# Kernel optimization log

Measured on AMD Instinct MI355X. Metric: run time of the kernel, lower is better.

Reference implementation:

```python
import jax, jax.numpy as jnp
import numpy as np

B, Z, A, D = 2048, 128, 4, 50000
EPS = 1e-8


def setup_inputs() -> dict:
    key = jax.random.key(0)
    k1, k2, k3, k4, k5 = jax.random.split(key, 5)
    return {
        "batch_x": jax.random.normal(k1, (B, Z), dtype=jnp.float32),
        "batch_next": jax.random.normal(k2, (B, Z), dtype=jnp.float32),
        "keys": jax.random.normal(k3, (A, D, Z), dtype=jnp.float32),
        "vals": jax.random.normal(k4, (A, D, Z), dtype=jnp.float32),
        "batch_a": jax.random.randint(k5, (B,), 0, A, dtype=jnp.int64),
    }


def _dnd_lookup(q, keys_a, vals_a):
    # q: [B, Z] (L2-normalized), keys_a: [D, Z], vals_a: [D, Z]
    kn = keys_a / (jnp.linalg.norm(keys_a, axis=-1, keepdims=True) + EPS)
    sims = jnp.einsum("bz,dz->bd", q, kn)          # cosine similarity [B, D]
    w = jax.nn.softmax(sims, axis=-1)                # attention over dictionary
    return jnp.einsum("bd,dz->bz", w, vals_a)       # [B, Z]


def reference(batch_x, batch_next, keys, vals, batch_a):
    # Per-sample routed DND lookup: each sample queries the memory of its action,
    # then MSE loss vs batch_next (eval-mode trainBatch; memory write is a state
    # mutation done after the loss and does not affect the returned value).
    qn = batch_x / (jnp.linalg.norm(batch_x, axis=-1, keepdims=True) + EPS)
    a_space = keys.shape[0]
    pred = jnp.zeros_like(batch_x)
    for a in range(a_space):  # small fixed loop over distinct memories
        pred_a = _dnd_lookup(qn, keys[a], vals[a])
        pred = jnp.where((batch_a == a)[:, None], pred_a, pred)
    return jnp.mean((pred - batch_next) ** 2)
```

## Files before the change

### kernel.cpp

```cpp
#include <hip/hip_runtime.h>
#include <stdint.h>

#define B_N 2048
#define Z_N 128
#define A_N 4
#define D_N 50000
#define EPS_F 1e-8f

typedef __attribute__((ext_vector_type(8))) short short8;
typedef __attribute__((ext_vector_type(4))) float f32x4;

__device__ __forceinline__ unsigned short f2bf(float f) {
  unsigned int u = __builtin_bit_cast(unsigned int, f);
  u += 0x7FFFu + ((u >> 16) & 1u);
  return (unsigned short)(u >> 16);
}

__global__ void k_qnorm_route(const float* __restrict__ x, const int* __restrict__ act,
                              float* __restrict__ qn, int* __restrict__ counts,
                              int* __restrict__ lists) {
  int w = threadIdx.x >> 6, lane = threadIdx.x & 63;
  int row = blockIdx.x * 4 + w;
  const float2 v = ((const float2*)(x + (size_t)row * Z_N))[lane];
  float ss = v.x * v.x + v.y * v.y;
#pragma unroll
  for (int m = 1; m < 64; m <<= 1) ss += __shfl_xor(ss, m);
  float inv = 1.0f / (sqrtf(ss) + EPS_F);
  float2 o; o.x = v.x * inv; o.y = v.y * inv;
  ((float2*)(qn + (size_t)row * Z_N))[lane] = o;
  if (lane == 0) {
    int a = act[row];
    int pos = atomicAdd(&counts[a], 1);
    lists[a * B_N + pos] = row;
  }
}

__global__ void k_keynorm(const float* __restrict__ keys, unsigned short* __restrict__ kn) {
  int w = threadIdx.x >> 6, lane = threadIdx.x & 63;
  size_t row = (size_t)blockIdx.x * 4 + w;
  const float2 v = ((const float2*)(keys + row * Z_N))[lane];
  float ss = v.x * v.x + v.y * v.y;
#pragma unroll
  for (int m = 1; m < 64; m <<= 1) ss += __shfl_xor(ss, m);
  float inv = 1.0f / (sqrtf(ss) + EPS_F);
  unsigned short2_t;
  unsigned int packed = ((unsigned int)f2bf(v.y * inv) << 16) | f2bf(v.x * inv);
  ((unsigned int*)(kn + row * Z_N))[lane] = packed;
}

__global__ void k_vtrans(const float* __restrict__ vals, unsigned short* __restrict__ vt) {
  __shared__ float tile[64][65];
  int a = blockIdx.z, d0 = blockIdx.x * 64, z0 = blockIdx.y * 64;
  int t = threadIdx.x;
  int r = t >> 4, c4 = (t & 15) * 4;
#pragma unroll
  for (int i = 0; i < 4; ++i) {
    int dr = r + i * 16, d = d0 + dr;
    if (d < D_N) {
      const float4 v = *(const float4*)(vals + ((size_t)a * D_N + d) * Z_N + z0 + c4);
      tile[dr][c4 + 0] = v.x; tile[dr][c4 + 1] = v.y;
      tile[dr][c4 + 2] = v.z; tile[dr][c4 + 3] = v.w;
    }
  }
  __syncthreads();
  int zz = t >> 2, dg = (t & 3) * 16;
  if (d0 + dg < D_N) {
    union { unsigned short u[16]; uint4 q[2]; } pk;
#pragma unroll
    for (int j = 0; j < 16; ++j) pk.u[j] = f2bf(tile[dg + j][zz]);
    unsigned short* dst = vt + ((size_t)a * Z_N + z0 + zz) * D_N + d0 + dg;
    ((uint4*)dst)[0] = pk.q[0];
    ((uint4*)dst)[1] = pk.q[1];
  }
}

#define TILE_B 128
#define KT 32
#define CHUNK 1568
#define NITER 49

__launch_bounds__(256, 2)
__global__ void k_flash(const unsigned short* __restrict__ kn,
                        const unsigned short* __restrict__ vt,
                        const float* __restrict__ qn,
                        const int* __restrict__ counts,
                        const int* __restrict__ lists,
                        float* __restrict__ acc,
                        float* __restrict__ sume) {
  int a = blockIdx.z, ty = blockIdx.y;
  int nb = counts[a];
  if (ty * TILE_B >= nb) return;

  __shared__ unsigned short Kl[KT * 136];
  __shared__ unsigned short Vl[128 * 40];
  __shared__ unsigned short Pl[4][32 * 40];

  int t = threadIdx.x;
  int w = t >> 6, lane = t & 63;
  int lq = lane >> 4, ln = lane & 15;

  const unsigned short* kn_a = kn + (size_t)a * D_N * Z_N;
  const unsigned short* vt_a = vt + (size_t)a * Z_N * D_N;
  const int* list_a = lists + a * B_N;

  short8 qf[2][4];
#pragma unroll
  for (int mt = 0; mt < 2; ++mt) {
    int g = ty * TILE_B + w * 32 + mt * 16 + ln;
    bool valid = g < nb;
    int si = valid ? list_a[g] : 0;
#pragma unroll
    for (int c = 0; c < 4; ++c) {
      float4 f0 = {0.f, 0.f, 0.f, 0.f}, f1 = {0.f, 0.f, 0.f, 0.f};
      if (valid) {
        const float* qp = qn + (size_t)si * Z_N + c * 32 + lq * 8;
        f0 = *(const float4*)qp;
        f1 = *(const float4*)(qp + 4);
      }
      short8 s;
      s[0] = (short)f2bf(f0.x); s[1] = (short)f2bf(f0.y);
      s[2] = (short)f2bf(f0.z); s[3] = (short)f2bf(f0.w);
      s[4] = (short)f2bf(f1.x); s[5] = (short)f2bf(f1.y);
      s[6] = (short)f2bf(f1.z); s[7] = (short)f2bf(f1.w);
      qf[mt][c] = s;
    }
  }

  f32x4 O[2][8];
#pragma unroll
  for (int mt = 0; mt < 2; ++mt)
#pragma unroll
    for (int zt = 0; zt < 8; ++zt) O[mt][zt] = (f32x4){0.f, 0.f, 0.f, 0.f};
  float rs[2][4] = {{0.f, 0.f, 0.f, 0.f}, {0.f, 0.f, 0.f, 0.f}};

  int d_base = blockIdx.x * CHUNK;
  int sk_key = t >> 3, sk_z = (t & 7) * 16;
  int sv_z = t >> 1, sv_k = (t & 1) * 16;

  for (int kt = 0; kt < NITER; ++kt) {
    int d0 = d_base + kt * KT;
    if (d0 >= D_N) break;
    __syncthreads();
    {
      int key = d0 + sk_key;
      if (key < D_N) {
        const uint4* src = (const uint4*)(kn_a + (size_t)key * Z_N + sk_z);
        uint4* dst = (uint4*)&Kl[sk_key * 136 + sk_z];
        dst[0] = src[0]; dst[1] = src[1];
      }
    }
    {
      int kk = d0 + sv_k;
      const unsigned short* src = vt_a + (size_t)sv_z * D_N + kk;
      uint4* dst = (uint4*)&Vl[sv_z * 40 + sv_k];
      if (kk < D_N)     dst[0] = *(const uint4*)src;
      if (kk + 8 < D_N) dst[1] = *(const uint4*)(src + 8);
    }
    __syncthreads();

    f32x4 S[2][2];
#pragma unroll
    for (int nt = 0; nt < 2; ++nt) {
      short8 kf[4];
#pragma unroll
      for (int c = 0; c < 4; ++c)
        kf[c] = *(const short8*)&Kl[(nt * 16 + ln) * 136 + c * 32 + lq * 8];
#pragma unroll
      for (int mt = 0; mt < 2; ++mt) {
        f32x4 s4 = (f32x4){0.f, 0.f, 0.f, 0.f};
#pragma unroll
        for (int c = 0; c < 4; ++c)
          s4 = __builtin_amdgcn_mfma_f32_16x16x32_bf16(qf[mt][c], kf[c], s4, 0, 0, 0);
        S[mt][nt] = s4;
      }
    }

#pragma unroll
    for (int mt = 0; mt < 2; ++mt)
#pragma unroll
      for (int nt = 0; nt < 2; ++nt) {
        bool kv = (d0 + nt * 16 + ln) < D_N;
#pragma unroll
        for (int r = 0; r < 4; ++r) {
          float e = kv ? __expf(S[mt][nt][r]) : 0.f;
          rs[mt][r] += e;
          Pl[w][(mt * 16 + lq * 4 + r) * 40 + nt * 16 + ln] = f2bf(e);
        }
      }

    short8 pf0 = *(const short8*)&Pl[w][(ln) * 40 + lq * 8];
    short8 pf1 = *(const short8*)&Pl[w][(16 + ln) * 40 + lq * 8];
#pragma unroll
    for (int zt = 0; zt < 8; ++zt) {
      short8 vf = *(const short8*)&Vl[(zt * 16 + ln) * 40 + lq * 8];
      O[0][zt] = __builtin_amdgcn_mfma_f32_16x16x32_bf16(pf0, vf, O[0][zt], 0, 0, 0);
      O[1][zt] = __builtin_amdgcn_mfma_f32_16x16x32_bf16(pf1, vf, O[1][zt], 0, 0, 0);
    }
  }

#pragma unroll
  for (int mt = 0; mt < 2; ++mt)
#pragma unroll
    for (int r = 0; r < 4; ++r) {
      float v = rs[mt][r];
      v += __shfl_xor(v, 1); v += __shfl_xor(v, 2);
      v += __shfl_xor(v, 4); v += __shfl_xor(v, 8);
      rs[mt][r] = v;
    }

#pragma unroll
  for (int mt = 0; mt < 2; ++mt)
#pragma unroll
    for (int r = 0; r < 4; ++r) {
      int g = ty * TILE_B + w * 32 + mt * 16 + lq * 4 + r;
      if (g < nb) {
        int si = list_a[g];
        float* arow = acc + (size_t)si * Z_N + ln;
#pragma unroll
        for (int zt = 0; zt < 8; ++zt) atomicAdd(arow + zt * 16, O[mt][zt][r]);
        if (ln == 0) atomicAdd(&sume[si], rs[mt][r]);
      }
    }
}

__global__ void k_loss(const float* __restrict__ acc, const float* __restrict__ sume,
                       const float* __restrict__ nxt, float* __restrict__ loss) {
  int w = threadIdx.x >> 6, lane = threadIdx.x & 63;
  int row = blockIdx.x * 4 + w;
  float inv = 1.0f / sume[row];
  const float2 p2 = ((const float2*)(acc + (size_t)row * Z_N))[lane];
  const float2 n2 = ((const float2*)(nxt + (size_t)row * Z_N))[lane];
  float dx = p2.x * inv - n2.x, dy = p2.y * inv - n2.y;
  float s = dx * dx + dy * dy;
#pragma unroll
  for (int m = 1; m < 64; m <<= 1) s += __shfl_xor(s, m);
  if (lane == 0) atomicAdd(loss, s);
}

__global__ void k_final(const float* __restrict__ loss, float* __restrict__ out) {
  out[0] = loss[0] * (1.0f / (float)(B_N * Z_N));
}

extern "C" void kernel_launch(void* const* d_in, const int* in_sizes, int n_in,
                              void* d_out, int out_size, void* d_ws, size_t ws_size,
                              hipStream_t stream) {
  const float* x    = (const float*)d_in[0];
  const float* nxt  = (const float*)d_in[1];
  const float* keys = (const float*)d_in[2];
  const float* vals = (const float*)d_in[3];
  const int*   act  = (const int*)d_in[4];

  char* ws = (char*)d_ws;
  float* qn     = (float*)(ws + 0);
  float* acc    = (float*)(ws + 1048576);
  float* sume   = (float*)(ws + 2097152);
  int*   counts = (int*)(ws + 2105344);
  float* loss   = (float*)(ws + 2105360);
  int*   lists  = (int*)(ws + 2105376);
  unsigned short* kn = (unsigned short*)(ws + 2138368);
  unsigned short* vt = (unsigned short*)(ws + 53338368);

  hipMemsetAsync(ws + 1048576, 0, 1056800, stream);

  k_qnorm_route<<<512, 256, 0, stream>>>(x, act, qn, counts, lists);
  k_keynorm<<<50000, 256, 0, stream>>>(keys, kn);
  k_vtrans<<<dim3(782, 2, A_N), 256, 0, stream>>>(vals, vt);
  k_flash<<<dim3(32, 16, A_N), 256, 0, stream>>>(kn, vt, qn, counts, lists, acc, sume);
  k_loss<<<512, 256, 0, stream>>>(acc, sume, nxt, loss);
  k_final<<<1, 1, 0, stream>>>(loss, (float*)d_out);
}
```

Before: 435.3 us.

## Prefetch next K/V tile into registers and split dictionary into smaller chunks

```diff
diff --git a/kernel.cpp b/kernel.cpp
--- a/kernel.cpp
+++ b/kernel.cpp
@@ -43,7 +43,6 @@
 #pragma unroll
   for (int m = 1; m < 64; m <<= 1) ss += __shfl_xor(ss, m);
   float inv = 1.0f / (sqrtf(ss) + EPS_F);
-  unsigned short2_t;
   unsigned int packed = ((unsigned int)f2bf(v.y * inv) << 16) | f2bf(v.x * inv);
   ((unsigned int*)(kn + row * Z_N))[lane] = packed;
 }
@@ -76,10 +75,11 @@
 
 #define TILE_B 128
 #define KT 32
-#define CHUNK 1568
-#define NITER 49
-
-__launch_bounds__(256, 2)
+#define CHUNK 800
+#define NITER 25
+#define NCHUNK 63
+
+__launch_bounds__(256, 4)
 __global__ void k_flash(const unsigned short* __restrict__ kn,
                         const unsigned short* __restrict__ vt,
                         const float* __restrict__ qn,
@@ -137,26 +137,43 @@
   int sk_key = t >> 3, sk_z = (t & 7) * 16;
   int sv_z = t >> 1, sv_k = (t & 1) * 16;
 
+  const uint4 z4 = {0u, 0u, 0u, 0u};
+  uint4 kA, kB, vA, vB;
+
+  {
+    int key = d_base + sk_key;
+    bool kok = key < D_N;
+    const uint4* ksrc = (const uint4*)(kn_a + (size_t)key * Z_N + sk_z);
+    kA = kok ? ksrc[0] : z4;
+    kB = kok ? ksrc[1] : z4;
+    int kk = d_base + sv_k;
+    const unsigned short* vsrc = vt_a + (size_t)sv_z * D_N + kk;
+    vA = (kk < D_N)     ? *(const uint4*)vsrc       : z4;
+    vB = (kk + 8 < D_N) ? *(const uint4*)(vsrc + 8) : z4;
+  }
+
   for (int kt = 0; kt < NITER; ++kt) {
     int d0 = d_base + kt * KT;
-    if (d0 >= D_N) break;
     __syncthreads();
     {
-      int key = d0 + sk_key;
-      if (key < D_N) {
-        const uint4* src = (const uint4*)(kn_a + (size_t)key * Z_N + sk_z);
-        uint4* dst = (uint4*)&Kl[sk_key * 136 + sk_z];
-        dst[0] = src[0]; dst[1] = src[1];
-      }
-    }
-    {
-      int kk = d0 + sv_k;
-      const unsigned short* src = vt_a + (size_t)sv_z * D_N + kk;
-      uint4* dst = (uint4*)&Vl[sv_z * 40 + sv_k];
-      if (kk < D_N)     dst[0] = *(const uint4*)src;
-      if (kk + 8 < D_N) dst[1] = *(const uint4*)(src + 8);
+      uint4* kd = (uint4*)&Kl[sk_key * 136 + sk_z];
+      kd[0] = kA; kd[1] = kB;
+      uint4* vd = (uint4*)&Vl[sv_z * 40 + sv_k];
+      vd[0] = vA; vd[1] = vB;
     }
     __syncthreads();
+    if (kt + 1 < NITER) {
+      int d1 = d0 + KT;
+      int key = d1 + sk_key;
+      bool kok = key < D_N;
+      const uint4* ksrc = (const uint4*)(kn_a + (size_t)key * Z_N + sk_z);
+      kA = kok ? ksrc[0] : z4;
+      kB = kok ? ksrc[1] : z4;
+      int kk = d1 + sv_k;
+      const unsigned short* vsrc = vt_a + (size_t)sv_z * D_N + kk;
+      vA = (kk < D_N)     ? *(const uint4*)vsrc       : z4;
+      vB = (kk + 8 < D_N) ? *(const uint4*)(vsrc + 8) : z4;
+    }
 
     f32x4 S[2][2];
 #pragma unroll
@@ -225,6 +242,7 @@
 
 __global__ void k_loss(const float* __restrict__ acc, const float* __restrict__ sume,
                        const float* __restrict__ nxt, float* __restrict__ loss) {
+  __shared__ float ls[4];
   int w = threadIdx.x >> 6, lane = threadIdx.x & 63;
   int row = blockIdx.x * 4 + w;
   float inv = 1.0f / sume[row];
@@ -234,7 +252,9 @@
   float s = dx * dx + dy * dy;
 #pragma unroll
   for (int m = 1; m < 64; m <<= 1) s += __shfl_xor(s, m);
-  if (lane == 0) atomicAdd(loss, s);
+  if (lane == 0) ls[w] = s;
+  __syncthreads();
+  if (threadIdx.x == 0) atomicAdd(loss, ls[0] + ls[1] + ls[2] + ls[3]);
 }
 
 __global__ void k_final(const float* __restrict__ loss, float* __restrict__ out) {
@@ -265,7 +285,7 @@
   k_qnorm_route<<<512, 256, 0, stream>>>(x, act, qn, counts, lists);
   k_keynorm<<<50000, 256, 0, stream>>>(keys, kn);
   k_vtrans<<<dim3(782, 2, A_N), 256, 0, stream>>>(vals, vt);
-  k_flash<<<dim3(32, 16, A_N), 256, 0, stream>>>(kn, vt, qn, counts, lists, acc, sume);
+  k_flash<<<dim3(NCHUNK, 16, A_N), 256, 0, stream>>>(kn, vt, qn, counts, lists, acc, sume);
   k_loss<<<512, 256, 0, stream>>>(acc, sume, nxt, loss);
   k_final<<<1, 1, 0, stream>>>(loss, (float*)d_out);
 }
```

Result: slower. 767.3 us (+76.3%).
